# Performance work log

Hardware: AMD Instinct MI355X
Metric: run time of the kernel (lower is better)

Reference implementation:

```python
import jax, jax.numpy as jnp
import numpy as np

DIM = 1024
NUM_HEADS = 16
HEAD_DIM = DIM // NUM_HEADS
SCALE = HEAD_DIM ** (-0.5)


def setup_inputs() -> dict:
    key = jax.random.key(0)
    ks = jax.random.split(key, 5)
    B, L, D = 2, 2048, DIM
    x = jax.random.normal(ks[0], (B, L, D), dtype=jnp.float32)
    # torch nn.Linear init scale ~ U(-1/sqrt(fan_in), 1/sqrt(fan_in)); use small normals
    s = 1.0 / np.sqrt(D)
    qkv_w = jax.random.uniform(ks[1], (3 * D, D), minval=-s, maxval=s, dtype=jnp.float32)
    qkv_b = jax.random.uniform(ks[2], (3 * D,), minval=-s, maxval=s, dtype=jnp.float32)
    proj_w = jax.random.uniform(ks[3], (D, D), minval=-s, maxval=s, dtype=jnp.float32)
    proj_b = jax.random.uniform(ks[4], (D,), minval=-s, maxval=s, dtype=jnp.float32)
    return {"x": x, "qkv_w": qkv_w, "qkv_b": qkv_b, "proj_w": proj_w, "proj_b": proj_b}


def reference(x, qkv_w, qkv_b, proj_w, proj_b):
    B, L, D = x.shape
    H, Hd = NUM_HEADS, HEAD_DIM
    # QKV projection: [B,L,3D] -> [3,B,H,L,Hd]
    qkv = x @ qkv_w.T + qkv_b
    qkv = qkv.reshape(B, L, 3, H, Hd).transpose(2, 0, 3, 1, 4)
    q, k, v = qkv[0], qkv[1], qkv[2]
    scores = jnp.einsum('bhqd,bhkd->bhqk', q, k) * SCALE  # [B,H,L,L]
    attn = jax.nn.softmax(scores, axis=-1)
    out = jnp.einsum('bhqk,bhkd->bhqd', attn, v)  # [B,H,L,Hd]
    out = out.transpose(0, 2, 1, 3).reshape(B, L, D)
    out = out @ proj_w.T + proj_b
    return out
```

## Files before the change

### kernel.cpp

```cpp
#include <hip/hip_runtime.h>
#include <hip/hip_bf16.h>
#include <cstdint>
#include <cstddef>

#define D_MODEL 1024
#define NHEADS 16
#define HD 64
#define NB 2
#define SL 2048
#define SEQ (NB*SL)
#define NQKV (3*D_MODEL)

typedef __attribute__((ext_vector_type(8))) short short8;
typedef __attribute__((ext_vector_type(4))) float floatx4;
typedef __attribute__((ext_vector_type(16))) float f32x16;
typedef unsigned short u16;

__device__ __forceinline__ u16 f2bf(float f) {
    union { float f; uint32_t u; } v; v.f = f;
    return (u16)((v.u + 0x7fffu + ((v.u >> 16) & 1u)) >> 16);
}

__device__ __forceinline__ uint32_t cvt_pk_bf16(float lo, float hi) {
    uint32_t r;
    asm("v_cvt_pk_bf16_f32 %0, %1, %2" : "=v"(r) : "v"(lo), "v"(hi));
    return r;
}

__device__ __forceinline__ void pl32swap(uint32_t &a, uint32_t &b) {
    asm("v_permlane32_swap_b32 %0, %1" : "+v"(a), "+v"(b));
}

__device__ __forceinline__ float exp2f_fast(float x) {
    float r; asm("v_exp_f32 %0, %1" : "=v"(r) : "v"(x)); return r;
}

__device__ __forceinline__ float m3f(float a, float b, float c) {
    return fmaxf(fmaxf(a, b), c);
}

__device__ __forceinline__ float vmax16(const f32x16& v) {
    float a0 = m3f(v[0], v[1], v[2]);
    float a1 = m3f(v[3], v[4], v[5]);
    float a2 = m3f(v[6], v[7], v[8]);
    float a3 = m3f(v[9], v[10], v[11]);
    float a4 = m3f(v[12], v[13], v[14]);
    return fmaxf(m3f(a0, a1, v[15]), m3f(a2, a3, a4));
}

__device__ __forceinline__ f32x16 zero16() {
    f32x16 z;
    #pragma unroll
    for (int i = 0; i < 16; i++) z[i] = 0.f;
    return z;
}

#define GLDS(gsrc, ldst) __builtin_amdgcn_global_load_lds( \
    (const __attribute__((address_space(1))) void*)(gsrc), \
    (__attribute__((address_space(3))) void*)(ldst), 16, 0, 0)

__global__ __launch_bounds__(256) void cvt_all(const float* __restrict__ x,
                                               const float* __restrict__ w1,
                                               const float* __restrict__ w2,
                                               u16* __restrict__ xb,
                                               u16* __restrict__ w1b,
                                               u16* __restrict__ w2b) {
    int i = blockIdx.x * 256 + threadIdx.x;
    const float4* src; ushort4* dst; int j;
    if (i < 1048576)      { src = (const float4*)x;  dst = (ushort4*)xb;  j = i; }
    else if (i < 1835008) { src = (const float4*)w1; dst = (ushort4*)w1b; j = i - 1048576; }
    else                  { src = (const float4*)w2; dst = (ushort4*)w2b; j = i - 1835008; }
    float4 f = src[j];
    ushort4 o;
    o.x = f2bf(f.x); o.y = f2bf(f.y); o.z = f2bf(f.z); o.w = f2bf(f.w);
    dst[j] = o;
}

__device__ __forceinline__ void gemm128x64_dbuf(const u16* __restrict__ A,
                                                const u16* __restrict__ B,
                                                int mbase, int nbase, int K,
                                                u16* Alds, u16* Blds,
                                                floatx4 acc[4][2]) {
    const int tid = threadIdx.x;
    const int lane = tid & 63;
    const int l15 = lane & 15, quad = lane >> 4;
    const int wave = tid >> 6;
    const int wr = wave >> 1, wc = wave & 1;
    #pragma unroll
    for (int i = 0; i < 4; i++)
        #pragma unroll
        for (int j = 0; j < 2; j++)
            acc[i][j] = (floatx4){0.f, 0.f, 0.f, 0.f};

    const int r0 = tid >> 2, kg0 = (tid & 3) * 8;
    const u16* Arow0 = A + (size_t)(mbase + r0) * K + kg0;
    const u16* Arow1 = A + (size_t)(mbase + r0 + 64) * K + kg0;
    const u16* Brow0 = B + (size_t)(nbase + r0) * K + kg0;

    GLDS(Arow0, Alds + tid * 8);
    GLDS(Arow1, Alds + (256 + tid) * 8);
    GLDS(Brow0, Blds + tid * 8);
    __syncthreads();

    const int NT = K >> 5;
    for (int t = 0; t < NT; t++) {
        const int cur = t & 1;
        if (t + 1 < NT) {
            const int k0 = (t + 1) << 5;
            u16* Ad = Alds + (cur ^ 1) * 4096;
            u16* Bd = Blds + (cur ^ 1) * 2048;
            GLDS(Arow0 + k0, Ad + tid * 8);
            GLDS(Arow1 + k0, Ad + (256 + tid) * 8);
            GLDS(Brow0 + k0, Bd + tid * 8);
        }
        const u16* Ac = Alds + cur * 4096;
        const u16* Bc = Blds + cur * 2048;
        short8 af[4], bf[2];
        #pragma unroll
        for (int i = 0; i < 4; i++)
            af[i] = *(const short8*)(Ac + (wr * 64 + i * 16 + l15) * 32 + quad * 8);
        #pragma unroll
        for (int j = 0; j < 2; j++)
            bf[j] = *(const short8*)(Bc + (wc * 32 + j * 16 + l15) * 32 + quad * 8);
        #pragma unroll
        for (int i = 0; i < 4; i++)
            #pragma unroll
            for (int j = 0; j < 2; j++)
                acc[i][j] = __builtin_amdgcn_mfma_f32_16x16x32_bf16(af[i], bf[j], acc[i][j], 0, 0, 0);
        __syncthreads();
    }
}

__global__ __launch_bounds__(256) void qkv_gemm(const u16* __restrict__ xb,
                                                const u16* __restrict__ wb,
                                                const float* __restrict__ bias,
                                                u16* __restrict__ Qo, u16* __restrict__ Ko,
                                                u16* __restrict__ Vt) {
    __shared__ __align__(16) u16 Alds[2 * 4096];
    __shared__ __align__(16) u16 Blds[2 * 2048];
    const int mbase = blockIdx.y * 128;
    const int nbase = blockIdx.x * 64;
    floatx4 acc[4][2];
    gemm128x64_dbuf(xb, wb, mbase, nbase, 1024, Alds, Blds, acc);
    const int lane = threadIdx.x & 63;
    const int wave = threadIdx.x >> 6;
    const int wr = wave >> 1, wc = wave & 1;
    const int l15 = lane & 15, quad = lane >> 4;
    const int which = nbase >> 10;
    #pragma unroll
    for (int j = 0; j < 2; j++) {
        int n = nbase + wc * 32 + j * 16 + l15;
        float bv = bias[n];
        int within = n & 1023;
        int h = within >> 6, d = within & 63;
        #pragma unroll
        for (int i = 0; i < 4; i++) {
            int m0 = mbase + wr * 64 + i * 16 + quad * 4;
            int b = m0 >> 11;
            int bh = b * NHEADS + h;
            if (which == 2) {
                int l0 = m0 & 2047;
                int slot = ((l0 >> 5) & 1) * 256 + ((l0 >> 4) & 1) * 128 + (d >> 5) * 64 + ((l0 >> 3) & 1) * 32 + (d & 31);
                ushort4 pk;
                pk.x = f2bf(acc[i][j][0] + bv); pk.y = f2bf(acc[i][j][1] + bv);
                pk.z = f2bf(acc[i][j][2] + bv); pk.w = f2bf(acc[i][j][3] + bv);
                *(ushort4*)(Vt + (size_t)bh * (SL * HD) + (size_t)(l0 >> 6) * 4096 + slot * 8 + (l0 & 7)) = pk;
            } else {
                #pragma unroll
                for (int r = 0; r < 4; r++) {
                    int m = m0 + r;
                    int l = m & 2047;
                    float v = acc[i][j][r] + bv;
                    if (which == 0) {
                        Qo[((size_t)bh * SL + l) * HD + d] = f2bf(v * 0.18033688f);
                    } else {
                        int slot = ((l >> 5) & 1) * 256 + (d >> 4) * 64 + ((d >> 3) & 1) * 32 + (l & 31);
                        Ko[(size_t)bh * (SL * HD) + (size_t)(l >> 6) * 4096 + slot * 8 + (d & 7)] = f2bf(v);
                    }
                }
            }
        }
    }
}

__global__ __launch_bounds__(512, 4) void flash_kernel(const u16* __restrict__ Q,
                                                       const u16* __restrict__ K,
                                                       const u16* __restrict__ V,
                                                       u16* __restrict__ AO) {
    __shared__ __align__(16) u16 smem[32768];
    const int tid = threadIdx.x;
    const int lane = tid & 63;
    const int wave = tid >> 6;
    const int qc = wave & 3;
    const int kvh = wave >> 2;
    const int tl = tid & 255;
    const int hi = lane >> 5;
    const int l31 = lane & 31;
    const int lane8 = lane * 8;

    const int bid = (int)blockIdx.x;
    const int swz = (bid & 7) * 64 + (bid >> 3);
    const int bh = swz >> 4;
    const int qb = swz & 15;
    const int b = bh >> 4, hd = bh & 15;
    const int qbase = qb * 128 + qc * 32;

    const u16* Qp = Q + (size_t)bh * SL * HD;
    const u16* Kg = K + (size_t)bh * (SL * HD) + (size_t)kvh * 16 * 4096;
    const u16* Vg = V + (size_t)bh * (SL * HD) + (size_t)kvh * 16 * 4096;

    u16* Kb_ = smem + kvh * 16384;
    u16* Vb_ = smem + kvh * 16384 + 8192;

    short8 qf[4];
    #pragma unroll
    for (int c = 0; c < 4; c++)
        qf[c] = *(const short8*)(Qp + (size_t)(qbase + l31) * HD + c * 16 + hi * 8);

    f32x16 accO0 = zero16(), accO1 = zero16();
    float m_i = -__builtin_inff();
    float l_i = 0.f;

    GLDS(Kg + tl * 8,         Kb_ + tl * 8);
    GLDS(Kg + (256 + tl) * 8, Kb_ + (256 + tl) * 8);
    GLDS(Vg + tl * 8,         Vb_ + tl * 8);
    GLDS(Vg + (256 + tl) * 8, Vb_ + (256 + tl) * 8);
    __syncthreads();

    union PW { uint32_t w[4]; short8 s8; };

    #pragma unroll 1
    for (int t = 0; t < 16; t++) {
        const int cur = t & 1;
        if (t + 1 < 16) {
            const u16* ks = Kg + (size_t)(t + 1) * 4096;
            const u16* vs = Vg + (size_t)(t + 1) * 4096;
            u16* kd = Kb_ + (cur ^ 1) * 4096;
            u16* vd = Vb_ + (cur ^ 1) * 4096;
            GLDS(ks + tl * 8,         kd + tl * 8);
            GLDS(ks + (256 + tl) * 8, kd + (256 + tl) * 8);
            GLDS(vs + tl * 8,         vd + tl * 8);
            GLDS(vs + (256 + tl) * 8, vd + (256 + tl) * 8);
        }
        const u16* Kt  = Kb_ + cur * 4096;
        const u16* Vt_ = Vb_ + cur * 4096;

        f32x16 sA = zero16(), sB = zero16();
        __builtin_amdgcn_s_setprio(1);
        #pragma unroll
        for (int c = 0; c < 4; c++) {
            short8 kf = *(const short8*)(Kt + c * 512 + lane8);
            sA = __builtin_amdgcn_mfma_f32_32x32x16_bf16(kf, qf[c], sA, 0, 0, 0);
        }
        #pragma unroll
        for (int c = 0; c < 4; c++) {
            short8 kf = *(const short8*)(Kt + 2048 + c * 512 + lane8);
            sB = __builtin_amdgcn_mfma_f32_32x32x16_bf16(kf, qf[c], sB, 0, 0, 0);
        }
        __builtin_amdgcn_s_setprio(0);

        float pmax = fmaxf(vmax16(sA), vmax16(sB));
        if (!__all(pmax - m_i <= 24.0f)) {
            float mo = m_i;
            float mn = fmaxf(mo, fmaxf(pmax, __shfl_xor(pmax, 32, 64)));
            m_i = mn;
            float alpha = exp2f_fast(mo - mn);
            l_i *= alpha;
            #pragma unroll
            for (int e = 0; e < 16; e++) { accO0[e] *= alpha; accO1[e] *= alpha; }
        }
        #pragma unroll
        for (int e = 0; e < 16; e++) sA[e] = exp2f_fast(sA[e] - m_i);
        #pragma unroll
        for (int e = 0; e < 16; e++) sB[e] = exp2f_fast(sB[e] - m_i);
        float r0 = 0.f, r1 = 0.f, r2 = 0.f, r3 = 0.f;
        #pragma unroll
        for (int e = 0; e < 16; e += 4) {
            r0 += sA[e]; r1 += sA[e + 1]; r2 += sA[e + 2]; r3 += sA[e + 3];
        }
        #pragma unroll
        for (int e = 0; e < 16; e += 4) {
            r0 += sB[e]; r1 += sB[e + 1]; r2 += sB[e + 2]; r3 += sB[e + 3];
        }
        float rs = (r0 + r1) + (r2 + r3);
        rs += __shfl_xor(rs, 32, 64);
        l_i += rs;

#define PV_SUB(SV, OFF) { \
        uint32_t a0 = cvt_pk_bf16(SV[0], SV[1]);  uint32_t b0 = cvt_pk_bf16(SV[4], SV[5]);  pl32swap(a0, b0); \
        uint32_t a1 = cvt_pk_bf16(SV[2], SV[3]);  uint32_t b1 = cvt_pk_bf16(SV[6], SV[7]);  pl32swap(a1, b1); \
        PW f0; f0.w[0] = a0; f0.w[1] = a1; f0.w[2] = b0; f0.w[3] = b1; \
        accO0 = __builtin_amdgcn_mfma_f32_32x32x16_bf16(*(const short8*)(Vt_ + (OFF) + lane8),        f0.s8, accO0, 0, 0, 0); \
        accO1 = __builtin_amdgcn_mfma_f32_32x32x16_bf16(*(const short8*)(Vt_ + (OFF) + 512 + lane8),  f0.s8, accO1, 0, 0, 0); \
        uint32_t c0 = cvt_pk_bf16(SV[8], SV[9]);  uint32_t d0 = cvt_pk_bf16(SV[12], SV[13]); pl32swap(c0, d0); \
        uint32_t c1 = cvt_pk_bf16(SV[10], SV[11]); uint32_t d1 = cvt_pk_bf16(SV[14], SV[15]); pl32swap(c1, d1); \
        PW f1; f1.w[0] = c0; f1.w[1] = c1; f1.w[2] = d0; f1.w[3] = d1; \
        accO0 = __builtin_amdgcn_mfma_f32_32x32x16_bf16(*(const short8*)(Vt_ + (OFF) + 1024 + lane8),       f1.s8, accO0, 0, 0, 0); \
        accO1 = __builtin_amdgcn_mfma_f32_32x32x16_bf16(*(const short8*)(Vt_ + (OFF) + 1024 + 512 + lane8), f1.s8, accO1, 0, 0, 0); }

        __builtin_amdgcn_s_setprio(1);
        PV_SUB(sA, 0);
        PV_SUB(sB, 2048);
        __builtin_amdgcn_s_setprio(0);
#undef PV_SUB

        __syncthreads();
    }

    float* xch = (float*)smem;
    if (kvh) {
        float* p = xch + (qc * 64 + lane) * 35;
        #pragma unroll
        for (int e = 0; e < 16; e++) { p[e] = accO0[e]; p[16 + e] = accO1[e]; }
        p[32] = m_i; p[33] = l_i;
    }
    __syncthreads();
    if (!kvh) {
        const float* p = xch + (qc * 64 + lane) * 35;
        float mB = p[32], lB = p[33];
        float m = fmaxf(m_i, mB);
        float s0 = exp2f_fast(m_i - m);
        float s1 = exp2f_fast(mB - m);
        float inv = 1.f / (s0 * l_i + s1 * lB);
        const size_t rowbase = ((size_t)(b * SL + qbase + l31)) * D_MODEL + hd * HD;
        #pragma unroll
        for (int rg = 0; rg < 4; rg++) {
            ushort4 o0, o1;
            o0.x = f2bf((s0 * accO0[rg * 4 + 0] + s1 * p[rg * 4 + 0]) * inv);
            o0.y = f2bf((s0 * accO0[rg * 4 + 1] + s1 * p[rg * 4 + 1]) * inv);
            o0.z = f2bf((s0 * accO0[rg * 4 + 2] + s1 * p[rg * 4 + 2]) * inv);
            o0.w = f2bf((s0 * accO0[rg * 4 + 3] + s1 * p[rg * 4 + 3]) * inv);
            *(ushort4*)(AO + rowbase + rg * 8 + 4 * hi) = o0;
            o1.x = f2bf((s0 * accO1[rg * 4 + 0] + s1 * p[16 + rg * 4 + 0]) * inv);
            o1.y = f2bf((s0 * accO1[rg * 4 + 1] + s1 * p[16 + rg * 4 + 1]) * inv);
            o1.z = f2bf((s0 * accO1[rg * 4 + 2] + s1 * p[16 + rg * 4 + 2]) * inv);
            o1.w = f2bf((s0 * accO1[rg * 4 + 3] + s1 * p[16 + rg * 4 + 3]) * inv);
            *(ushort4*)(AO + rowbase + 32 + rg * 8 + 4 * hi) = o1;
        }
    }
}

__global__ __launch_bounds__(256) void proj_gemm(const u16* __restrict__ ab,
                                                 const u16* __restrict__ wb,
                                                 const float* __restrict__ bias,
                                                 float* __restrict__ out) {
    __shared__ __align__(16) u16 Alds[2 * 4096];
    __shared__ __align__(16) u16 Blds[2 * 2048];
    const int mbase = blockIdx.y * 128;
    const int nbase = blockIdx.x * 64;
    floatx4 acc[4][2];
    gemm128x64_dbuf(ab, wb, mbase, nbase, 1024, Alds, Blds, acc);
    const int lane = threadIdx.x & 63;
    const int wave = threadIdx.x >> 6;
    const int wr = wave >> 1, wc = wave & 1;
    const int l15 = lane & 15, quad = lane >> 4;
    #pragma unroll
    for (int j = 0; j < 2; j++) {
        int n = nbase + wc * 32 + j * 16 + l15;
        float bv = bias[n];
        #pragma unroll
        for (int i = 0; i < 4; i++) {
            #pragma unroll
            for (int r = 0; r < 4; r++) {
                int m = mbase + wr * 64 + i * 16 + quad * 4 + r;
                out[(size_t)m * D_MODEL + n] = acc[i][j][r] + bv;
            }
        }
    }
}

extern "C" void kernel_launch(void* const* d_in, const int* in_sizes, int n_in,
                              void* d_out, int out_size, void* d_ws, size_t ws_size,
                              hipStream_t stream) {
    const float* x      = (const float*)d_in[0];
    const float* qkv_w  = (const float*)d_in[1];
    const float* qkv_b  = (const float*)d_in[2];
    const float* proj_w = (const float*)d_in[3];
    const float* proj_b = (const float*)d_in[4];
    float* out = (float*)d_out;
    char* ws = (char*)d_ws;

    u16* xb    = (u16*)(ws);
    u16* wqkv  = (u16*)(ws + 8388608);
    u16* wproj = (u16*)(ws + 14680064);
    u16* Qb    = (u16*)(ws + 16777216);
    u16* Kb    = (u16*)(ws + 25165824);
    u16* Vt    = (u16*)(ws + 33554432);
    u16* AO    = (u16*)(ws);

    cvt_all<<<8192, 256, 0, stream>>>(x, qkv_w, proj_w, xb, wqkv, wproj);
    qkv_gemm<<<dim3(NQKV / 64, SEQ / 128), 256, 0, stream>>>(xb, wqkv, qkv_b, Qb, Kb, Vt);
    flash_kernel<<<dim3(512), 512, 0, stream>>>(Qb, Kb, Vt, AO);
    proj_gemm<<<dim3(D_MODEL / 64, SEQ / 128), 256, 0, stream>>>(AO, wproj, proj_b, out);
}
```

Baseline: 199.3 us.

## Rewrite QKV GEMM as 256x256 tile with direct-to-LDS staged ping-pong pipeline

The QKV projection GEMM moves from 128x64 tiles with 256 threads to 256x256 tiles with 512 threads. Operands are staged with global-to-LDS loads into double buffers and interleaved with MFMA sub-blocks, using barriers and priority hints. The aim is more reuse of each loaded tile and better overlap of memory traffic with MFMA work. The grid shrinks to 12x16=192 blocks, which may leave some CUs idle, and the larger accumulator set raises register pressure. Separately, the flash kernel now does its cross-half row-sum shuffle once after the KV loop rather than on every iteration.

```diff
diff --git a/kernel.cpp b/kernel.cpp
--- a/kernel.cpp
+++ b/kernel.cpp
@@ -131,46 +131,136 @@
     }
 }
 
-__global__ __launch_bounds__(256) void qkv_gemm(const u16* __restrict__ xb,
-                                                const u16* __restrict__ wb,
-                                                const float* __restrict__ bias,
-                                                u16* __restrict__ Qo, u16* __restrict__ Ko,
-                                                u16* __restrict__ Vt) {
-    __shared__ __align__(16) u16 Alds[2 * 4096];
-    __shared__ __align__(16) u16 Blds[2 * 2048];
-    const int mbase = blockIdx.y * 128;
-    const int nbase = blockIdx.x * 64;
-    floatx4 acc[4][2];
-    gemm128x64_dbuf(xb, wb, mbase, nbase, 1024, Alds, Blds, acc);
-    const int lane = threadIdx.x & 63;
-    const int wave = threadIdx.x >> 6;
-    const int wr = wave >> 1, wc = wave & 1;
+
+#define QMFMA(MOFF, NOFF) \
+    _Pragma("unroll") for (int mf_ = 0; mf_ < 4; mf_++) \
+    _Pragma("unroll") for (int nf_ = 0; nf_ < 2; nf_++) \
+    _Pragma("unroll") for (int kk_ = 0; kk_ < 2; kk_++) \
+        acc[(MOFF)+mf_][(NOFF)+nf_] = __builtin_amdgcn_mfma_f32_16x16x32_bf16( \
+            af[mf_][kk_], bf[(NOFF)+nf_][kk_], acc[(MOFF)+mf_][(NOFF)+nf_], 0, 0, 0);
+
+#define KSTEP(CA, CB, NA, NB_, KCOL, DOSTAGE) {                                  \
+    _Pragma("unroll") for (int mf_ = 0; mf_ < 4; mf_++)                          \
+      _Pragma("unroll") for (int kk_ = 0; kk_ < 2; kk_++)                        \
+        af[mf_][kk_] = *(const short8*)((CA) + ArdB + (mf_*2+kk_)*512);          \
+    _Pragma("unroll") for (int nf_ = 0; nf_ < 2; nf_++)                          \
+      _Pragma("unroll") for (int kk_ = 0; kk_ < 2; kk_++)                        \
+        bf[nf_][kk_] = *(const short8*)((CB) + BrdB + (nf_*2+kk_)*512);          \
+    if (DOSTAGE) {                                                               \
+      _Pragma("unroll") for (int r_ = 0; r_ < 4; r_++)                           \
+        GLDS(srcA[r_] + (KCOL), (NA) + dOff[r_]);                                \
+    }                                                                            \
+    __builtin_amdgcn_s_barrier();                                                \
+    __builtin_amdgcn_s_setprio(1);                                               \
+    QMFMA(0, 0)                                                                  \
+    __builtin_amdgcn_s_setprio(0);                                               \
+    __builtin_amdgcn_s_barrier();                                                \
+    _Pragma("unroll") for (int nf_ = 0; nf_ < 2; nf_++)                          \
+      _Pragma("unroll") for (int kk_ = 0; kk_ < 2; kk_++)                        \
+        bf[2+nf_][kk_] = *(const short8*)((CB) + BrdB + ((2+nf_)*2+kk_)*512);    \
+    if (DOSTAGE) {                                                               \
+      _Pragma("unroll") for (int r_ = 0; r_ < 4; r_++)                           \
+        GLDS(srcB[r_] + (KCOL), (NB_) + dOff[r_]);                               \
+    }                                                                            \
+    __builtin_amdgcn_s_barrier();                                                \
+    __builtin_amdgcn_s_setprio(1);                                               \
+    QMFMA(0, 2)                                                                  \
+    __builtin_amdgcn_s_setprio(0);                                               \
+    __builtin_amdgcn_s_barrier();                                                \
+    _Pragma("unroll") for (int mf_ = 0; mf_ < 4; mf_++)                          \
+      _Pragma("unroll") for (int kk_ = 0; kk_ < 2; kk_++)                        \
+        af[mf_][kk_] = *(const short8*)((CA) + ArdB + ((4+mf_)*2+kk_)*512);      \
+    __builtin_amdgcn_s_barrier();                                                \
+    __builtin_amdgcn_s_setprio(1);                                               \
+    QMFMA(4, 2)                                                                  \
+    __builtin_amdgcn_s_setprio(0);                                               \
+    __builtin_amdgcn_s_barrier();                                                \
+    __builtin_amdgcn_s_setprio(1);                                               \
+    QMFMA(4, 0)                                                                  \
+    __builtin_amdgcn_s_setprio(0);                                               \
+    asm volatile("s_waitcnt vmcnt(0)" ::: "memory");                             \
+    __builtin_amdgcn_s_barrier();                                                \
+}
+
+__global__ __launch_bounds__(512, 2) void qkv_gemm(const u16* __restrict__ xb,
+                                                   const u16* __restrict__ wb,
+                                                   const float* __restrict__ bias,
+                                                   u16* __restrict__ Qo, u16* __restrict__ Ko,
+                                                   u16* __restrict__ Vt) {
+    __shared__ __align__(16) u16 smem[65536];
+    const int tid = threadIdx.x;
+    const int lane = tid & 63;
+    const int wave = tid >> 6;
+    const int wr = wave >> 2, wc = wave & 3;
     const int l15 = lane & 15, quad = lane >> 4;
+    const int mbase = blockIdx.y * 256;
+    const int nbase = blockIdx.x * 256;
+
+    const u16* srcA[4]; const u16* srcB[4]; int dOff[4];
+    #pragma unroll
+    for (int r = 0; r < 4; r++) {
+        int s = r * 512 + tid;
+        int mm = s >> 7, kk = (s >> 6) & 1, qs = (s >> 4) & 3, ls = s & 15;
+        srcA[r] = xb + (size_t)(mbase + mm * 16 + ls) * 1024 + kk * 32 + qs * 8;
+        srcB[r] = wb + (size_t)(nbase + mm * 16 + ls) * 1024 + kk * 32 + qs * 8;
+        dOff[r] = s * 8;
+    }
+    u16* const A0 = smem;
+    u16* const A1 = smem + 16384;
+    u16* const B0 = smem + 32768;
+    u16* const B1 = smem + 49152;
+
+    const int ArdB = wr * 8192 + lane * 8;
+    const int BrdB = wc * 4096 + lane * 8;
+
+    floatx4 acc[8][4];
+    #pragma unroll
+    for (int i = 0; i < 8; i++)
+        #pragma unroll
+        for (int j = 0; j < 4; j++)
+            acc[i][j] = (floatx4){0.f, 0.f, 0.f, 0.f};
+    short8 af[4][2], bf[4][2];
+
+    #pragma unroll
+    for (int r = 0; r < 4; r++) GLDS(srcA[r], A0 + dOff[r]);
+    #pragma unroll
+    for (int r = 0; r < 4; r++) GLDS(srcB[r], B0 + dOff[r]);
+    asm volatile("s_waitcnt vmcnt(0)" ::: "memory");
+    __builtin_amdgcn_s_barrier();
+
+    #pragma unroll 1
+    for (int tt = 0; tt < 8; tt++) {
+        const int kc1 = (tt * 2 + 1) * 64;
+        const int kc2 = (tt * 2 + 2) * 64;
+        KSTEP(A0, B0, A1, B1, kc1, true)
+        KSTEP(A1, B1, A0, B0, kc2, (tt < 7))
+    }
+
     const int which = nbase >> 10;
     #pragma unroll
-    for (int j = 0; j < 2; j++) {
-        int n = nbase + wc * 32 + j * 16 + l15;
+    for (int nf = 0; nf < 4; nf++) {
+        int n = nbase + wc * 64 + nf * 16 + l15;
         float bv = bias[n];
         int within = n & 1023;
         int h = within >> 6, d = within & 63;
         #pragma unroll
-        for (int i = 0; i < 4; i++) {
-            int m0 = mbase + wr * 64 + i * 16 + quad * 4;
+        for (int mf = 0; mf < 8; mf++) {
+            int m0 = mbase + wr * 128 + mf * 16 + quad * 4;
             int b = m0 >> 11;
             int bh = b * NHEADS + h;
             if (which == 2) {
                 int l0 = m0 & 2047;
                 int slot = ((l0 >> 5) & 1) * 256 + ((l0 >> 4) & 1) * 128 + (d >> 5) * 64 + ((l0 >> 3) & 1) * 32 + (d & 31);
                 ushort4 pk;
-                pk.x = f2bf(acc[i][j][0] + bv); pk.y = f2bf(acc[i][j][1] + bv);
-                pk.z = f2bf(acc[i][j][2] + bv); pk.w = f2bf(acc[i][j][3] + bv);
+                pk.x = f2bf(acc[mf][nf][0] + bv); pk.y = f2bf(acc[mf][nf][1] + bv);
+                pk.z = f2bf(acc[mf][nf][2] + bv); pk.w = f2bf(acc[mf][nf][3] + bv);
                 *(ushort4*)(Vt + (size_t)bh * (SL * HD) + (size_t)(l0 >> 6) * 4096 + slot * 8 + (l0 & 7)) = pk;
             } else {
                 #pragma unroll
                 for (int r = 0; r < 4; r++) {
                     int m = m0 + r;
                     int l = m & 2047;
-                    float v = acc[i][j][r] + bv;
+                    float v = acc[mf][nf][r] + bv;
                     if (which == 0) {
                         Qo[((size_t)bh * SL + l) * HD + d] = f2bf(v * 0.18033688f);
                     } else {
@@ -282,9 +372,7 @@
         for (int e = 0; e < 16; e += 4) {
             r0 += sB[e]; r1 += sB[e + 1]; r2 += sB[e + 2]; r3 += sB[e + 3];
         }
-        float rs = (r0 + r1) + (r2 + r3);
-        rs += __shfl_xor(rs, 32, 64);
-        l_i += rs;
+        l_i += (r0 + r1) + (r2 + r3);
 
 #define PV_SUB(SV, OFF) { \
         uint32_t a0 = cvt_pk_bf16(SV[0], SV[1]);  uint32_t b0 = cvt_pk_bf16(SV[4], SV[5]);  pl32swap(a0, b0); \
@@ -306,6 +394,8 @@
 
         __syncthreads();
     }
+
+    l_i += __shfl_xor(l_i, 32, 64);
 
     float* xch = (float*)smem;
     if (kvh) {
@@ -389,7 +479,7 @@
     u16* AO    = (u16*)(ws);
 
     cvt_all<<<8192, 256, 0, stream>>>(x, qkv_w, proj_w, xb, wqkv, wproj);
-    qkv_gemm<<<dim3(NQKV / 64, SEQ / 128), 256, 0, stream>>>(xb, wqkv, qkv_b, Qb, Kb, Vt);
+    qkv_gemm<<<dim3(NQKV / 256, SEQ / 256), 512, 0, stream>>>(xb, wqkv, qkv_b, Qb, Kb, Vt);
     flash_kernel<<<dim3(512), 512, 0, stream>>>(Qb, Kb, Vt, AO);
     proj_gemm<<<dim3(D_MODEL / 64, SEQ / 128), 256, 0, stream>>>(AO, wproj, proj_b, out);
 }
```

Measured after the change: 196.5 us. About the same (-1.4%).
